# Kernel optimization log

Measured on AMD Instinct MI355X. Metric: run time of the kernel, lower is better.

Reference implementation:

```python
import jax, jax.numpy as jnp
import numpy as np

N_NODES = 10000
IN_CH = 512
HID = 128
HEADS = 4
OUT_CH = 256
N_EDGES = 160000
NEG_SLOPE = 0.2  # PyG GATConv default


def gat_conv(x, src, dst, W, a_src, a_dst, b):
    """PyG-style GATConv. x:[N,F_in], W:[F_in,H*C], a_src/a_dst:[H,C], b:[H*C].
    src/dst already include self-loops. Returns [N, H*C] (concat heads)."""
    N = x.shape[0]
    H, C = a_src.shape
    h = (x @ W).reshape(N, H, C)                     # [N,H,C]
    e_src = jnp.einsum('nhc,hc->nh', h, a_src)        # [N,H]
    e_dst = jnp.einsum('nhc,hc->nh', h, a_dst)
    alpha = jax.nn.leaky_relu(e_src[src] + e_dst[dst], NEG_SLOPE)  # [E,H]
    # softmax over incoming edges of each destination node
    m = jax.ops.segment_max(alpha, dst, num_segments=N)            # [N,H]
    ex = jnp.exp(alpha - m[dst])
    denom = jax.ops.segment_sum(ex, dst, num_segments=N)           # [N,H]
    coeff = ex / (denom[dst] + 1e-16)                              # [E,H]
    out = jax.ops.segment_sum(coeff[:, :, None] * h[src], dst, num_segments=N)  # [N,H,C]
    return out.reshape(N, H * C) + b


def _edges_with_self_loops(edge_index, n):
    loops = jnp.arange(n, dtype=edge_index.dtype)
    src = jnp.concatenate([edge_index[0], loops])
    dst = jnp.concatenate([edge_index[1], loops])
    return src, dst


def setup_inputs() -> dict:
    key = jax.random.key(0)
    ks = jax.random.split(key, 20)
    s = 0.05
    inp = {
        'x': jax.random.normal(ks[0], (N_NODES, IN_CH), jnp.float32),
        'W1': jax.random.normal(ks[1], (IN_CH, HEADS * HID), jnp.float32) * s,
        'a1s': jax.random.normal(ks[2], (HEADS, HID), jnp.float32) * s,
        'a1d': jax.random.normal(ks[3], (HEADS, HID), jnp.float32) * s,
        'b1': jnp.zeros((HEADS * HID,), jnp.float32),
        'W2': jax.random.normal(ks[4], (HEADS * HID, HEADS * HID), jnp.float32) * s,
        'a2s': jax.random.normal(ks[5], (HEADS, HID), jnp.float32) * s,
        'a2d': jax.random.normal(ks[6], (HEADS, HID), jnp.float32) * s,
        'b2': jnp.zeros((HEADS * HID,), jnp.float32),
        'W3': jax.random.normal(ks[7], (HEADS * HID, HID), jnp.float32) * s,
        'a3s': jax.random.normal(ks[8], (1, HID), jnp.float32) * s,
        'a3d': jax.random.normal(ks[9], (1, HID), jnp.float32) * s,
        'b3': jnp.zeros((HID,), jnp.float32),
        'Wl': jax.random.normal(ks[10], (HID, OUT_CH), jnp.float32) * s,
        'bl': jnp.zeros((OUT_CH,), jnp.float32),
        'Wr': jax.random.normal(ks[11], (IN_CH, OUT_CH), jnp.float32) * s,
        'br': jnp.zeros((OUT_CH,), jnp.float32),
        'edge_index': jax.random.randint(ks[12], (2, N_EDGES), 0, N_NODES, jnp.int64 if jax.config.jax_enable_x64 else jnp.int32),
    }
    return inp


def reference(x, W1, a1s, a1d, b1, W2, a2s, a2d, b2, W3, a3s, a3d, b3, Wl, bl, Wr, br, edge_index):
    src, dst = _edges_with_self_loops(edge_index, x.shape[0])
    residual = x @ Wr + br
    h = jax.nn.elu(gat_conv(x, src, dst, W1, a1s, a1d, b1))
    h = jax.nn.elu(gat_conv(h, src, dst, W2, a2s, a2d, b2))
    h = jax.nn.elu(gat_conv(h, src, dst, W3, a3s, a3d, b3))
    return h @ Wl + bl + residual
```

## Files before the change

### kernel.cpp

```cpp
#include <hip/hip_runtime.h>
#include <hip/hip_bf16.h>
#include <cstdint>
#include <cstddef>

#define N_NODES 10000
#define M_PAD   10112
#define HEADS   4

typedef __bf16 bfrag8 __attribute__((ext_vector_type(8)));
typedef __bf16 bfrag2 __attribute__((ext_vector_type(2)));
typedef float  floatx4 __attribute__((ext_vector_type(4)));

#define S0 (M_PAD * 512)
#define S1 (512 * 512)
#define S2 (512 * 512)
#define S3 (512 * 128)
#define S4 (128 * 256)
#define S5 (512 * 256)
#define SP_TOTAL (S0 + S1 + S2 + S3 + S4 + S5 + N_NODES)

__global__ __launch_bounds__(256) void prep(const float* __restrict__ x,
                                            const float* __restrict__ W1,
                                            const float* __restrict__ W2,
                                            const float* __restrict__ W3,
                                            const float* __restrict__ Wl,
                                            const float* __restrict__ Wr,
                                            __bf16* __restrict__ xb,
                                            __bf16* __restrict__ W1T,
                                            __bf16* __restrict__ W2T,
                                            __bf16* __restrict__ W3T,
                                            __bf16* __restrict__ WlT,
                                            __bf16* __restrict__ WrT,
                                            int* __restrict__ deg) {
    int i = blockIdx.x * 256 + threadIdx.x;
    if (i < S0) {
        int row = i >> 9;
        xb[i] = (row < N_NODES) ? (__bf16)x[i] : (__bf16)0.f;
    } else if ((i -= S0) < S1) {
        int k = i >> 9, n = i & 511;
        W1T[n * 512 + k] = (__bf16)W1[i];
    } else if ((i -= S1) < S2) {
        int k = i >> 9, n = i & 511;
        W2T[n * 512 + k] = (__bf16)W2[i];
    } else if ((i -= S2) < S3) {
        int k = i >> 7, n = i & 127;
        W3T[n * 512 + k] = (__bf16)W3[i];
    } else if ((i -= S3) < S4) {
        int k = i >> 8, n = i & 255;
        WlT[n * 128 + k] = (__bf16)Wl[i];
    } else if ((i -= S4) < S5) {
        int k = i >> 8, n = i & 255;
        WrT[n * 512 + k] = (__bf16)Wr[i];
    } else if ((i -= S5) < N_NODES) {
        deg[i] = 0;
    }
}


__global__ __launch_bounds__(256) void deg_kernel(const int* __restrict__ dst, int E,
                                                  int* __restrict__ deg) {
    int i = blockIdx.x * 256 + threadIdx.x;
    if (i < E) atomicAdd(&deg[dst[i]], 1);
}

__global__ __launch_bounds__(256) void scan_kernel(const int* __restrict__ deg,
                                                   int* __restrict__ rowptr,
                                                   int* __restrict__ cursor, int n) {
    __shared__ int wtot[4], woff[4];
    int t = threadIdx.x, lane = t & 63, wv = t >> 6;
    int chunk = (n + 255) / 256;
    int beg = t * chunk, end = beg + chunk; if (end > n) end = n; if (beg > n) beg = n;
    int s = 0;
    for (int i = beg; i < end; ++i) s += deg[i] + 1;
    int v = s;
#pragma unroll
    for (int off = 1; off < 64; off <<= 1) {
        int o = __shfl_up(v, off);
        if (lane >= off) v += o;
    }
    if (lane == 63) wtot[wv] = v;
    __syncthreads();
    if (t == 0) {
        int r = 0;
#pragma unroll
        for (int i = 0; i < 4; ++i) { woff[i] = r; r += wtot[i]; }
        rowptr[n] = r;
    }
    __syncthreads();
    int off = woff[wv] + v - s;
    for (int i = beg; i < end; ++i) {
        rowptr[i] = off; cursor[i] = off;
        off += deg[i] + 1;
    }
}

__global__ __launch_bounds__(256) void scatter_kernel(const int* __restrict__ src,
                                                      const int* __restrict__ dst, int E, int n,
                                                      int* __restrict__ cursor,
                                                      int* __restrict__ csr) {
    int i = blockIdx.x * 256 + threadIdx.x;
    if (i < E) {
        int pos = atomicAdd(&cursor[dst[i]], 1);
        csr[pos] = src[i];
    } else if (i < E + n) {
        int v = i - E;
        int pos = atomicAdd(&cursor[v], 1);
        csr[pos] = v;
    }
}


template <int NT>
__device__ __forceinline__ void gemm_loop(const __bf16* __restrict__ A,
                                          const __bf16* __restrict__ BT, int K,
                                          int m0, int n0, int wave, int lane,
                                          __bf16* As, __bf16* Bs,
                                          floatx4 (&acc)[2][NT]) {
    int r = wave * 8 + (lane >> 3);
    int kof = (lane & 7) * 8;
    const __bf16* gA = A + (size_t)(m0 + r) * K + kof;
    const __bf16* gB = BT + (size_t)(n0 + r) * K + kof;
    __bf16* lA = As + r * 64 + kof;
    __bf16* lB = Bs + r * 64 + kof;
    const __bf16* fA = As + (wave * 32 + (lane & 15)) * 64 + (lane >> 4) * 8;
    const __bf16* fB = Bs + (lane & 15) * 64 + (lane >> 4) * 8;

    for (int k0 = 0; k0 < K; k0 += 64) {
#pragma unroll
        for (int u = 0; u < 4; ++u)
            __builtin_amdgcn_global_load_lds(
                (const __attribute__((address_space(1))) void*)(gA + (size_t)u * 32 * K),
                (__attribute__((address_space(3))) void*)(lA + u * 32 * 64), 16, 0, 0);
#pragma unroll
        for (int u = 0; u < NT / 2; ++u)
            __builtin_amdgcn_global_load_lds(
                (const __attribute__((address_space(1))) void*)(gB + (size_t)u * 32 * K),
                (__attribute__((address_space(3))) void*)(lB + u * 32 * 64), 16, 0, 0);
        gA += 64; gB += 64;
        __syncthreads();

#pragma unroll
        for (int ks = 0; ks < 2; ++ks) {
            bfrag8 a0 = *(const bfrag8*)(fA + ks * 32);
            bfrag8 a1 = *(const bfrag8*)(fA + 16 * 64 + ks * 32);
#pragma unroll
            for (int nt = 0; nt < NT; ++nt) {
                bfrag8 b = *(const bfrag8*)(fB + nt * 16 * 64 + ks * 32);
                acc[0][nt] = __builtin_amdgcn_mfma_f32_16x16x32_bf16(a0, b, acc[0][nt], 0, 0, 0);
                acc[1][nt] = __builtin_amdgcn_mfma_f32_16x16x32_bf16(a1, b, acc[1][nt], 0, 0, 0);
            }
        }
        __syncthreads();
    }
}

__global__ __launch_bounds__(256) void gemm_h(const __bf16* __restrict__ A,
                                              const __bf16* __restrict__ BT,
                                              __bf16* __restrict__ Cb,
                                              int N, int K) {
    __shared__ __align__(16) __bf16 As[128 * 64];
    __shared__ __align__(16) __bf16 Bs[64 * 64];
    int tid = threadIdx.x, wave = tid >> 6, lane = tid & 63;
    int m0 = blockIdx.x * 128, n0 = blockIdx.y * 64;
    floatx4 acc[2][4] = {};
    gemm_loop<4>(A, BT, K, m0, n0, wave, lane, As, Bs, acc);

    int crow = m0 + wave * 32 + (lane >> 4) * 4;
    int ccol = n0 + (lane & 15);
#pragma unroll
    for (int mt = 0; mt < 2; ++mt)
#pragma unroll
        for (int nt = 0; nt < 4; ++nt)
#pragma unroll
            for (int r = 0; r < 4; ++r)
                Cb[(size_t)(crow + mt * 16 + r) * N + ccol + nt * 16] = (__bf16)acc[mt][nt][r];
}

__global__ __launch_bounds__(256) void gemm_final(const __bf16* __restrict__ A1,
                                                  const __bf16* __restrict__ B1T, int K1,
                                                  const __bf16* __restrict__ A2,
                                                  const __bf16* __restrict__ B2T, int K2,
                                                  float* __restrict__ C,
                                                  const float* __restrict__ bias1,
                                                  const float* __restrict__ bias2,
                                                  int M, int N) {
    __shared__ __align__(16) __bf16 As[128 * 64];
    __shared__ __align__(16) __bf16 Bs[64 * 64];
    int tid = threadIdx.x, wave = tid >> 6, lane = tid & 63;
    int m0 = blockIdx.x * 128, n0 = blockIdx.y * 64;
    floatx4 acc[2][4] = {};
    gemm_loop<4>(A1, B1T, K1, m0, n0, wave, lane, As, Bs, acc);
    gemm_loop<4>(A2, B2T, K2, m0, n0, wave, lane, As, Bs, acc);

    int crow = m0 + wave * 32 + (lane >> 4) * 4;
    int ccol = n0 + (lane & 15);
#pragma unroll
    for (int mt = 0; mt < 2; ++mt)
#pragma unroll
        for (int nt = 0; nt < 4; ++nt)
#pragma unroll
            for (int r = 0; r < 4; ++r) {
                int row = crow + mt * 16 + r;
                int col = ccol + nt * 16;
                if (row < M)
                    C[(size_t)row * N + col] = acc[mt][nt][r] + bias1[col] + bias2[col];
            }
}


template <int H>
__global__ __launch_bounds__(256) void attn_e(const __bf16* __restrict__ Hb,
                                              const float* __restrict__ as_,
                                              const float* __restrict__ ad_,
                                              float* __restrict__ es,
                                              float* __restrict__ ed) {
    constexpr int F = H * 128;
    constexpr int GROUP = (H == 4) ? 16 : 64;
    int wave = threadIdx.x >> 6, lane = threadIdx.x & 63;
    int node = blockIdx.x * 4 + wave;
    if (node >= N_NODES) return;
    float ps = 0.f, pd = 0.f;
    if (H == 4) {
        bfrag8 v = *(const bfrag8*)(Hb + (size_t)node * F + lane * 8);
#pragma unroll
        for (int k = 0; k < 8; ++k) {
            float f = (float)v[k];
            ps += f * as_[lane * 8 + k];
            pd += f * ad_[lane * 8 + k];
        }
    } else {
        bfrag2 v = *(const bfrag2*)(Hb + (size_t)node * F + lane * 2);
#pragma unroll
        for (int k = 0; k < 2; ++k) {
            float f = (float)v[k];
            ps += f * as_[lane * 2 + k];
            pd += f * ad_[lane * 2 + k];
        }
    }
#pragma unroll
    for (int off = GROUP / 2; off; off >>= 1) {
        ps += __shfl_down(ps, off);
        pd += __shfl_down(pd, off);
    }
    if ((lane & (GROUP - 1)) == 0) {
        es[node * H + lane / GROUP] = ps;
        ed[node * H + lane / GROUP] = pd;
    }
}


template <int H>
__global__ __launch_bounds__(256) void gather_agg(const __bf16* __restrict__ Hb,
                                                  const float* __restrict__ es,
                                                  const float* __restrict__ ed,
                                                  const int* __restrict__ rowptr,
                                                  const int* __restrict__ csr,
                                                  const float* __restrict__ bias,
                                                  __bf16* __restrict__ outb) {
    constexpr int F = H * 128;
    constexpr int CH = F / 64;
    int wave = threadIdx.x >> 6, lane = threadIdx.x & 63;
    int node = blockIdx.x * 4 + wave;
    if (node >= M_PAD) return;
    int hsel = (H == 4) ? (lane >> 4) : 0;
    __bf16* op = outb + (size_t)node * F + lane * CH;
    if (node >= N_NODES) {
        if (H == 4) { bfrag8 z = {}; *(bfrag8*)op = z; }
        else        { bfrag2 z = {}; *(bfrag2*)op = z; }
        return;
    }
    float edv = ed[node * H + hsel];
    int beg = rowptr[node], end = rowptr[node + 1];
    float acc[CH] = {};
    float wsum = 0.f;
    int j = beg;
    for (; j + 3 < end; j += 4) {
        int s0 = csr[j], s1 = csr[j + 1], s2 = csr[j + 2], s3 = csr[j + 3];
        float e0 = es[s0 * H + hsel], e1 = es[s1 * H + hsel];
        float e2 = es[s2 * H + hsel], e3 = es[s3 * H + hsel];
        if (H == 4) {
            bfrag8 h0 = *(const bfrag8*)(Hb + (size_t)s0 * F + lane * 8);
            bfrag8 h1 = *(const bfrag8*)(Hb + (size_t)s1 * F + lane * 8);
            bfrag8 h2 = *(const bfrag8*)(Hb + (size_t)s2 * F + lane * 8);
            bfrag8 h3 = *(const bfrag8*)(Hb + (size_t)s3 * F + lane * 8);
            e0 += edv; e1 += edv; e2 += edv; e3 += edv;
            e0 = e0 > 0.f ? e0 : 0.2f * e0;
            e1 = e1 > 0.f ? e1 : 0.2f * e1;
            e2 = e2 > 0.f ? e2 : 0.2f * e2;
            e3 = e3 > 0.f ? e3 : 0.2f * e3;
            float w0 = __expf(e0), w1 = __expf(e1), w2 = __expf(e2), w3 = __expf(e3);
            wsum += (w0 + w1) + (w2 + w3);
#pragma unroll
            for (int k = 0; k < 8; ++k)
                acc[k] += (w0 * (float)h0[k] + w1 * (float)h1[k]) +
                          (w2 * (float)h2[k] + w3 * (float)h3[k]);
        } else {
            bfrag2 h0 = *(const bfrag2*)(Hb + (size_t)s0 * F + lane * 2);
            bfrag2 h1 = *(const bfrag2*)(Hb + (size_t)s1 * F + lane * 2);
            bfrag2 h2 = *(const bfrag2*)(Hb + (size_t)s2 * F + lane * 2);
            bfrag2 h3 = *(const bfrag2*)(Hb + (size_t)s3 * F + lane * 2);
            e0 += edv; e1 += edv; e2 += edv; e3 += edv;
            e0 = e0 > 0.f ? e0 : 0.2f * e0;
            e1 = e1 > 0.f ? e1 : 0.2f * e1;
            e2 = e2 > 0.f ? e2 : 0.2f * e2;
            e3 = e3 > 0.f ? e3 : 0.2f * e3;
            float w0 = __expf(e0), w1 = __expf(e1), w2 = __expf(e2), w3 = __expf(e3);
            wsum += (w0 + w1) + (w2 + w3);
#pragma unroll
            for (int k = 0; k < 2; ++k)
                acc[k] += (w0 * (float)h0[k] + w1 * (float)h1[k]) +
                          (w2 * (float)h2[k] + w3 * (float)h3[k]);
        }
    }
    for (; j < end; ++j) {
        int s0 = csr[j];
        float e0 = es[s0 * H + hsel] + edv;
        e0 = e0 > 0.f ? e0 : 0.2f * e0;
        float w0 = __expf(e0);
        wsum += w0;
        if (H == 4) {
            bfrag8 h0 = *(const bfrag8*)(Hb + (size_t)s0 * F + lane * 8);
#pragma unroll
            for (int k = 0; k < 8; ++k) acc[k] += w0 * (float)h0[k];
        } else {
            bfrag2 h0 = *(const bfrag2*)(Hb + (size_t)s0 * F + lane * 2);
#pragma unroll
            for (int k = 0; k < 2; ++k) acc[k] += w0 * (float)h0[k];
        }
    }
    float inv = 1.f / (wsum + 1e-16f);
    if (H == 4) {
        bfrag8 r;
#pragma unroll
        for (int k = 0; k < 8; ++k) {
            float o = acc[k] * inv + bias[lane * 8 + k];
            o = o > 0.f ? o : __expf(o) - 1.f;
            r[k] = (__bf16)o;
        }
        *(bfrag8*)op = r;
    } else {
        bfrag2 r;
#pragma unroll
        for (int k = 0; k < 2; ++k) {
            float o = acc[k] * inv + bias[lane * 2 + k];
            o = o > 0.f ? o : __expf(o) - 1.f;
            r[k] = (__bf16)o;
        }
        *(bfrag2*)op = r;
    }
}


extern "C" void kernel_launch(void* const* d_in, const int* in_sizes, int n_in,
                              void* d_out, int out_size, void* d_ws, size_t ws_size,
                              hipStream_t stream) {
    const float* x   = (const float*)d_in[0];
    const float* W1  = (const float*)d_in[1];
    const float* a1s = (const float*)d_in[2];
    const float* a1d = (const float*)d_in[3];
    const float* b1  = (const float*)d_in[4];
    const float* W2  = (const float*)d_in[5];
    const float* a2s = (const float*)d_in[6];
    const float* a2d = (const float*)d_in[7];
    const float* b2  = (const float*)d_in[8];
    const float* W3  = (const float*)d_in[9];
    const float* a3s = (const float*)d_in[10];
    const float* a3d = (const float*)d_in[11];
    const float* b3  = (const float*)d_in[12];
    const float* Wl  = (const float*)d_in[13];
    const float* bl  = (const float*)d_in[14];
    const float* Wr  = (const float*)d_in[15];
    const float* br  = (const float*)d_in[16];
    const int*   ei  = (const int*)d_in[17];
    const int E = in_sizes[17] / 2;
    const int* esrc = ei;
    const int* edst = ei + E;
    const int slots = E + N_NODES;
    float* out = (float*)d_out;

    char* w = (char*)d_ws;
    auto alloc = [&](size_t b) { char* p = w; w += (b + 255) & ~(size_t)255; return p; };
    __bf16* xb  = (__bf16*)alloc((size_t)M_PAD * 512 * 2);
    __bf16* hb  = (__bf16*)alloc((size_t)M_PAD * 512 * 2);
    __bf16* hb3 = (__bf16*)alloc((size_t)M_PAD * 128 * 2);
    __bf16* Hib = (__bf16*)alloc((size_t)M_PAD * 512 * 2);
    __bf16* W1T = (__bf16*)alloc(512 * 512 * 2);
    __bf16* W2T = (__bf16*)alloc(512 * 512 * 2);
    __bf16* W3T = (__bf16*)alloc(128 * 512 * 2);
    __bf16* WlT = (__bf16*)alloc(256 * 128 * 2);
    __bf16* WrT = (__bf16*)alloc(256 * 512 * 2);
    float* es     = (float*)alloc(N_NODES * HEADS * 4);
    float* ed     = (float*)alloc(N_NODES * HEADS * 4);
    int*   deg    = (int*)alloc(N_NODES * 4);
    int*   rowptr = (int*)alloc((N_NODES + 1) * 4);
    int*   cursor = (int*)alloc(N_NODES * 4);
    int*   csr    = (int*)alloc((size_t)slots * 4);

    prep<<<(SP_TOTAL + 255) / 256, 256, 0, stream>>>(x, W1, W2, W3, Wl, Wr,
                                                     xb, W1T, W2T, W3T, WlT, WrT, deg);
    deg_kernel<<<(E + 255) / 256, 256, 0, stream>>>(edst, E, deg);
    scan_kernel<<<1, 256, 0, stream>>>(deg, rowptr, cursor, N_NODES);
    scatter_kernel<<<(E + N_NODES + 255) / 256, 256, 0, stream>>>(esrc, edst, E, N_NODES,
                                                                  cursor, csr);

    gemm_h<<<dim3(M_PAD / 128, 8), 256, 0, stream>>>(xb, W1T, Hib, 512, 512);
    attn_e<4><<<N_NODES / 4, 256, 0, stream>>>(Hib, a1s, a1d, es, ed);
    gather_agg<4><<<M_PAD / 4, 256, 0, stream>>>(Hib, es, ed, rowptr, csr, b1, hb);
    gemm_h<<<dim3(M_PAD / 128, 8), 256, 0, stream>>>(hb, W2T, Hib, 512, 512);
    attn_e<4><<<N_NODES / 4, 256, 0, stream>>>(Hib, a2s, a2d, es, ed);
    gather_agg<4><<<M_PAD / 4, 256, 0, stream>>>(Hib, es, ed, rowptr, csr, b2, hb);
    gemm_h<<<dim3(M_PAD / 128, 2), 256, 0, stream>>>(hb, W3T, Hib, 128, 512);
    attn_e<1><<<N_NODES / 4, 256, 0, stream>>>(Hib, a3s, a3d, es, ed);
    gather_agg<1><<<M_PAD / 4, 256, 0, stream>>>(Hib, es, ed, rowptr, csr, b3, hb3);
    gemm_final<<<dim3(M_PAD / 128, 4), 256, 0, stream>>>(xb, WrT, 512, hb3, WlT, 128,
                                                         out, br, bl, N_NODES, 256);
}
```

Before: 289.7 us.

## Fuse attention logits into GEMM epilogue, widen GEMM tiles, vectorize prep, unroll gather

Each GEMM block now covers a full 128-column head tile and computes the per-head source and destination attention logits in its epilogue with a shuffle reduction. This removes the separate attn_e kernels and their re-read of H. GEMM tiles widen from 64 to 128 columns and the grid is reordered so columns vary fastest. The x-to-bf16 conversion now converts 8 elements per thread with vector loads, and the gather loop unrolls 8 edges to keep more loads in flight. Larger accumulators raise register pressure, and the wider tiles give fewer blocks per GEMM.

```diff
diff --git a/kernel.cpp b/kernel.cpp
--- a/kernel.cpp
+++ b/kernel.cpp
@@ -11,13 +11,13 @@
 typedef __bf16 bfrag2 __attribute__((ext_vector_type(2)));
 typedef float  floatx4 __attribute__((ext_vector_type(4)));
 
-#define S0 (M_PAD * 512)
+#define S0V (M_PAD * 512 / 8)
 #define S1 (512 * 512)
 #define S2 (512 * 512)
 #define S3 (512 * 128)
 #define S4 (128 * 256)
 #define S5 (512 * 256)
-#define SP_TOTAL (S0 + S1 + S2 + S3 + S4 + S5 + N_NODES)
+#define SP_TOTAL (S0V + S1 + S2 + S3 + S4 + S5 + N_NODES)
 
 __global__ __launch_bounds__(256) void prep(const float* __restrict__ x,
                                             const float* __restrict__ W1,
@@ -33,10 +33,18 @@
                                             __bf16* __restrict__ WrT,
                                             int* __restrict__ deg) {
     int i = blockIdx.x * 256 + threadIdx.x;
-    if (i < S0) {
-        int row = i >> 9;
-        xb[i] = (row < N_NODES) ? (__bf16)x[i] : (__bf16)0.f;
-    } else if ((i -= S0) < S1) {
+    if (i < S0V) {
+        int base = i * 8;
+        int row = base >> 9;
+        bfrag8 r = {};
+        if (row < N_NODES) {
+            float4 f0 = ((const float4*)x)[i * 2];
+            float4 f1 = ((const float4*)x)[i * 2 + 1];
+            r[0] = (__bf16)f0.x; r[1] = (__bf16)f0.y; r[2] = (__bf16)f0.z; r[3] = (__bf16)f0.w;
+            r[4] = (__bf16)f1.x; r[5] = (__bf16)f1.y; r[6] = (__bf16)f1.z; r[7] = (__bf16)f1.w;
+        }
+        *(bfrag8*)(xb + base) = r;
+    } else if ((i -= S0V) < S1) {
         int k = i >> 9, n = i & 511;
         W1T[n * 512 + k] = (__bf16)W1[i];
     } else if ((i -= S1) < S2) {
@@ -157,23 +165,60 @@
 __global__ __launch_bounds__(256) void gemm_h(const __bf16* __restrict__ A,
                                               const __bf16* __restrict__ BT,
                                               __bf16* __restrict__ Cb,
-                                              int N, int K) {
+                                              int N, int K,
+                                              const float* __restrict__ as_,
+                                              const float* __restrict__ ad_,
+                                              float* __restrict__ es,
+                                              float* __restrict__ ed, int H) {
     __shared__ __align__(16) __bf16 As[128 * 64];
-    __shared__ __align__(16) __bf16 Bs[64 * 64];
+    __shared__ __align__(16) __bf16 Bs[128 * 64];
     int tid = threadIdx.x, wave = tid >> 6, lane = tid & 63;
-    int m0 = blockIdx.x * 128, n0 = blockIdx.y * 64;
-    floatx4 acc[2][4] = {};
-    gemm_loop<4>(A, BT, K, m0, n0, wave, lane, As, Bs, acc);
+    int n0 = blockIdx.x * 128, m0 = blockIdx.y * 128;
+    floatx4 acc[2][8] = {};
+    gemm_loop<8>(A, BT, K, m0, n0, wave, lane, As, Bs, acc);
 
     int crow = m0 + wave * 32 + (lane >> 4) * 4;
     int ccol = n0 + (lane & 15);
 #pragma unroll
     for (int mt = 0; mt < 2; ++mt)
 #pragma unroll
-        for (int nt = 0; nt < 4; ++nt)
+        for (int nt = 0; nt < 8; ++nt)
 #pragma unroll
             for (int r = 0; r < 4; ++r)
                 Cb[(size_t)(crow + mt * 16 + r) * N + ccol + nt * 16] = (__bf16)acc[mt][nt][r];
+
+    int head = blockIdx.x;
+    float a_sv[8], a_dv[8];
+#pragma unroll
+    for (int nt = 0; nt < 8; ++nt) {
+        int cin = nt * 16 + (lane & 15);
+        a_sv[nt] = as_[head * 128 + cin];
+        a_dv[nt] = ad_[head * 128 + cin];
+    }
+#pragma unroll
+    for (int mt = 0; mt < 2; ++mt)
+#pragma unroll
+        for (int r = 0; r < 4; ++r) {
+            float ps = 0.f, pd = 0.f;
+#pragma unroll
+            for (int nt = 0; nt < 8; ++nt) {
+                float v = acc[mt][nt][r];
+                ps += v * a_sv[nt];
+                pd += v * a_dv[nt];
+            }
+#pragma unroll
+            for (int off = 8; off; off >>= 1) {
+                ps += __shfl_xor(ps, off);
+                pd += __shfl_xor(pd, off);
+            }
+            if ((lane & 15) == 0) {
+                int row = crow + mt * 16 + r;
+                if (row < N_NODES) {
+                    es[row * H + head] = ps;
+                    ed[row * H + head] = pd;
+                }
+            }
+        }
 }
 
 __global__ __launch_bounds__(256) void gemm_final(const __bf16* __restrict__ A1,
@@ -185,19 +230,19 @@
                                                   const float* __restrict__ bias2,
                                                   int M, int N) {
     __shared__ __align__(16) __bf16 As[128 * 64];
-    __shared__ __align__(16) __bf16 Bs[64 * 64];
+    __shared__ __align__(16) __bf16 Bs[128 * 64];
     int tid = threadIdx.x, wave = tid >> 6, lane = tid & 63;
-    int m0 = blockIdx.x * 128, n0 = blockIdx.y * 64;
-    floatx4 acc[2][4] = {};
-    gemm_loop<4>(A1, B1T, K1, m0, n0, wave, lane, As, Bs, acc);
-    gemm_loop<4>(A2, B2T, K2, m0, n0, wave, lane, As, Bs, acc);
+    int n0 = blockIdx.x * 128, m0 = blockIdx.y * 128;
+    floatx4 acc[2][8] = {};
+    gemm_loop<8>(A1, B1T, K1, m0, n0, wave, lane, As, Bs, acc);
+    gemm_loop<8>(A2, B2T, K2, m0, n0, wave, lane, As, Bs, acc);
 
     int crow = m0 + wave * 32 + (lane >> 4) * 4;
     int ccol = n0 + (lane & 15);
 #pragma unroll
     for (int mt = 0; mt < 2; ++mt)
 #pragma unroll
-        for (int nt = 0; nt < 4; ++nt)
+        for (int nt = 0; nt < 8; ++nt)
 #pragma unroll
             for (int r = 0; r < 4; ++r) {
                 int row = crow + mt * 16 + r;
@@ -205,47 +250,6 @@
                 if (row < M)
                     C[(size_t)row * N + col] = acc[mt][nt][r] + bias1[col] + bias2[col];
             }
-}
-
-
-template <int H>
-__global__ __launch_bounds__(256) void attn_e(const __bf16* __restrict__ Hb,
-                                              const float* __restrict__ as_,
-                                              const float* __restrict__ ad_,
-                                              float* __restrict__ es,
-                                              float* __restrict__ ed) {
-    constexpr int F = H * 128;
-    constexpr int GROUP = (H == 4) ? 16 : 64;
-    int wave = threadIdx.x >> 6, lane = threadIdx.x & 63;
-    int node = blockIdx.x * 4 + wave;
-    if (node >= N_NODES) return;
-    float ps = 0.f, pd = 0.f;
-    if (H == 4) {
-        bfrag8 v = *(const bfrag8*)(Hb + (size_t)node * F + lane * 8);
-#pragma unroll
-        for (int k = 0; k < 8; ++k) {
-            float f = (float)v[k];
-            ps += f * as_[lane * 8 + k];
-            pd += f * ad_[lane * 8 + k];
-        }
-    } else {
-        bfrag2 v = *(const bfrag2*)(Hb + (size_t)node * F + lane * 2);
-#pragma unroll
-        for (int k = 0; k < 2; ++k) {
-            float f = (float)v[k];
-            ps += f * as_[lane * 2 + k];
-            pd += f * ad_[lane * 2 + k];
-        }
-    }
-#pragma unroll
-    for (int off = GROUP / 2; off; off >>= 1) {
-        ps += __shfl_down(ps, off);
-        pd += __shfl_down(pd, off);
-    }
-    if ((lane & (GROUP - 1)) == 0) {
-        es[node * H + lane / GROUP] = ps;
-        ed[node * H + lane / GROUP] = pd;
-    }
 }
 
 
@@ -274,42 +278,43 @@
     float acc[CH] = {};
     float wsum = 0.f;
     int j = beg;
-    for (; j + 3 < end; j += 4) {
-        int s0 = csr[j], s1 = csr[j + 1], s2 = csr[j + 2], s3 = csr[j + 3];
-        float e0 = es[s0 * H + hsel], e1 = es[s1 * H + hsel];
-        float e2 = es[s2 * H + hsel], e3 = es[s3 * H + hsel];
+    for (; j + 7 < end; j += 8) {
+        int s[8];
+        float e[8];
+#pragma unroll
+        for (int u = 0; u < 8; ++u) s[u] = csr[j + u];
+#pragma unroll
+        for (int u = 0; u < 8; ++u) e[u] = es[s[u] * H + hsel];
         if (H == 4) {
-            bfrag8 h0 = *(const bfrag8*)(Hb + (size_t)s0 * F + lane * 8);
-            bfrag8 h1 = *(const bfrag8*)(Hb + (size_t)s1 * F + lane * 8);
-            bfrag8 h2 = *(const bfrag8*)(Hb + (size_t)s2 * F + lane * 8);
-            bfrag8 h3 = *(const bfrag8*)(Hb + (size_t)s3 * F + lane * 8);
-            e0 += edv; e1 += edv; e2 += edv; e3 += edv;
-            e0 = e0 > 0.f ? e0 : 0.2f * e0;
-            e1 = e1 > 0.f ? e1 : 0.2f * e1;
-            e2 = e2 > 0.f ? e2 : 0.2f * e2;
-            e3 = e3 > 0.f ? e3 : 0.2f * e3;
-            float w0 = __expf(e0), w1 = __expf(e1), w2 = __expf(e2), w3 = __expf(e3);
-            wsum += (w0 + w1) + (w2 + w3);
-#pragma unroll
-            for (int k = 0; k < 8; ++k)
-                acc[k] += (w0 * (float)h0[k] + w1 * (float)h1[k]) +
-                          (w2 * (float)h2[k] + w3 * (float)h3[k]);
+            bfrag8 hv[8];
+#pragma unroll
+            for (int u = 0; u < 8; ++u) hv[u] = *(const bfrag8*)(Hb + (size_t)s[u] * F + lane * 8);
+#pragma unroll
+            for (int u = 0; u < 8; ++u) {
+                float t = e[u] + edv;
+                t = t > 0.f ? t : 0.2f * t;
+                e[u] = __expf(t);
+                wsum += e[u];
+            }
+#pragma unroll
+            for (int u = 0; u < 8; ++u)
+#pragma unroll
+                for (int k = 0; k < 8; ++k) acc[k] += e[u] * (float)hv[u][k];
         } else {
-            bfrag2 h0 = *(const bfrag2*)(Hb + (size_t)s0 * F + lane * 2);
-            bfrag2 h1 = *(const bfrag2*)(Hb + (size_t)s1 * F + lane * 2);
-            bfrag2 h2 = *(const bfrag2*)(Hb + (size_t)s2 * F + lane * 2);
-            bfrag2 h3 = *(const bfrag2*)(Hb + (size_t)s3 * F + lane * 2);
-            e0 += edv; e1 += edv; e2 += edv; e3 += edv;
-            e0 = e0 > 0.f ? e0 : 0.2f * e0;
-            e1 = e1 > 0.f ? e1 : 0.2f * e1;
-            e2 = e2 > 0.f ? e2 : 0.2f * e2;
-            e3 = e3 > 0.f ? e3 : 0.2f * e3;
-            float w0 = __expf(e0), w1 = __expf(e1), w2 = __expf(e2), w3 = __expf(e3);
-            wsum += (w0 + w1) + (w2 + w3);
-#pragma unroll
-            for (int k = 0; k < 2; ++k)
-                acc[k] += (w0 * (float)h0[k] + w1 * (float)h1[k]) +
-                          (w2 * (float)h2[k] + w3 * (float)h3[k]);
+            bfrag2 hv[8];
+#pragma unroll
+            for (int u = 0; u < 8; ++u) hv[u] = *(const bfrag2*)(Hb + (size_t)s[u] * F + lane * 2);
+#pragma unroll
+            for (int u = 0; u < 8; ++u) {
+                float t = e[u] + edv;
+                t = t > 0.f ? t : 0.2f * t;
+                e[u] = __expf(t);
+                wsum += e[u];
+            }
+#pragma unroll
+            for (int u = 0; u < 8; ++u)
+#pragma unroll
+                for (int k = 0; k < 2; ++k) acc[k] += e[u] * (float)hv[u][k];
         }
     }
     for (; j < end; ++j) {
@@ -403,15 +408,15 @@
     scatter_kernel<<<(E + N_NODES + 255) / 256, 256, 0, stream>>>(esrc, edst, E, N_NODES,
                                                                   cursor, csr);
 
-    gemm_h<<<dim3(M_PAD / 128, 8), 256, 0, stream>>>(xb, W1T, Hib, 512, 512);
-    attn_e<4><<<N_NODES / 4, 256, 0, stream>>>(Hib, a1s, a1d, es, ed);
+    gemm_h<<<dim3(4, M_PAD / 128), 256, 0, stream>>>(xb, W1T, Hib, 512, 512,
+                                                     a1s, a1d, es, ed, 4);
     gather_agg<4><<<M_PAD / 4, 256, 0, stream>>>(Hib, es, ed, rowptr, csr, b1, hb);
-    gemm_h<<<dim3(M_PAD / 128, 8), 256, 0, stream>>>(hb, W2T, Hib, 512, 512);
-    attn_e<4><<<N_NODES / 4, 256, 0, stream>>>(Hib, a2s, a2d, es, ed);
+    gemm_h<<<dim3(4, M_PAD / 128), 256, 0, stream>>>(hb, W2T, Hib, 512, 512,
+                                                     a2s, a2d, es, ed, 4);
     gather_agg<4><<<M_PAD / 4, 256, 0, stream>>>(Hib, es, ed, rowptr, csr, b2, hb);
-    gemm_h<<<dim3(M_PAD / 128, 2), 256, 0, stream>>>(hb, W3T, Hib, 128, 512);
-    attn_e<1><<<N_NODES / 4, 256, 0, stream>>>(Hib, a3s, a3d, es, ed);
+    gemm_h<<<dim3(1, M_PAD / 128), 256, 0, stream>>>(hb, W3T, Hib, 128, 512,
+                                                     a3s, a3d, es, ed, 1);
     gather_agg<1><<<M_PAD / 4, 256, 0, stream>>>(Hib, es, ed, rowptr, csr, b3, hb3);
-    gemm_final<<<dim3(M_PAD / 128, 4), 256, 0, stream>>>(xb, WrT, 512, hb3, WlT, 128,
+    gemm_final<<<dim3(2, M_PAD / 128), 256, 0, stream>>>(xb, WrT, 512, hb3, WlT, 128,
                                                          out, br, bl, N_NODES, 256);
 }
```

After: 292.3 us. About the same (+0.9%).

## Split gather per head, swap GEMM grid order, vectorize x conversion

Applied to the files above, without the earlier changes.

The 4-head neighbour aggregation is split into four separate launches, one per head. Each wave gathers 256 bytes per neighbour row (bf16x2 per lane), with 8 neighbours unrolled to keep more loads in flight. This is meant to shrink each launch's working set so it fits in cache. The GEMM grids now put the N-tile dimension on blockIdx.x so blocks sharing an A row-tile run close together, and the x-to-bf16 conversion in prep now uses float4 loads and 16-byte stores. The cost is more kernel launches, and the CSR and es data are re-read once per head.

```diff
diff --git a/kernel.cpp b/kernel.cpp
--- a/kernel.cpp
+++ b/kernel.cpp
@@ -11,13 +11,13 @@
 typedef __bf16 bfrag2 __attribute__((ext_vector_type(2)));
 typedef float  floatx4 __attribute__((ext_vector_type(4)));
 
-#define S0 (M_PAD * 512)
+#define S0V (M_PAD * 512 / 8)
 #define S1 (512 * 512)
 #define S2 (512 * 512)
 #define S3 (512 * 128)
 #define S4 (128 * 256)
 #define S5 (512 * 256)
-#define SP_TOTAL (S0 + S1 + S2 + S3 + S4 + S5 + N_NODES)
+#define SP_TOTAL (S0V + S1 + S2 + S3 + S4 + S5 + N_NODES)
 
 __global__ __launch_bounds__(256) void prep(const float* __restrict__ x,
                                             const float* __restrict__ W1,
@@ -33,10 +33,18 @@
                                             __bf16* __restrict__ WrT,
                                             int* __restrict__ deg) {
     int i = blockIdx.x * 256 + threadIdx.x;
-    if (i < S0) {
-        int row = i >> 9;
-        xb[i] = (row < N_NODES) ? (__bf16)x[i] : (__bf16)0.f;
-    } else if ((i -= S0) < S1) {
+    if (i < S0V) {
+        int base = i * 8;
+        int row = base >> 9;
+        bfrag8 r = {};
+        if (row < N_NODES) {
+            float4 f0 = ((const float4*)x)[i * 2];
+            float4 f1 = ((const float4*)x)[i * 2 + 1];
+            r[0] = (__bf16)f0.x; r[1] = (__bf16)f0.y; r[2] = (__bf16)f0.z; r[3] = (__bf16)f0.w;
+            r[4] = (__bf16)f1.x; r[5] = (__bf16)f1.y; r[6] = (__bf16)f1.z; r[7] = (__bf16)f1.w;
+        }
+        *(bfrag8*)(xb + base) = r;
+    } else if ((i -= S0V) < S1) {
         int k = i >> 9, n = i & 511;
         W1T[n * 512 + k] = (__bf16)W1[i];
     } else if ((i -= S1) < S2) {
@@ -161,7 +169,7 @@
     __shared__ __align__(16) __bf16 As[128 * 64];
     __shared__ __align__(16) __bf16 Bs[64 * 64];
     int tid = threadIdx.x, wave = tid >> 6, lane = tid & 63;
-    int m0 = blockIdx.x * 128, n0 = blockIdx.y * 64;
+    int n0 = blockIdx.x * 64, m0 = blockIdx.y * 128;
     floatx4 acc[2][4] = {};
     gemm_loop<4>(A, BT, K, m0, n0, wave, lane, As, Bs, acc);
 
@@ -187,7 +195,7 @@
     __shared__ __align__(16) __bf16 As[128 * 64];
     __shared__ __align__(16) __bf16 Bs[64 * 64];
     int tid = threadIdx.x, wave = tid >> 6, lane = tid & 63;
-    int m0 = blockIdx.x * 128, n0 = blockIdx.y * 64;
+    int n0 = blockIdx.x * 64, m0 = blockIdx.y * 128;
     floatx4 acc[2][4] = {};
     gemm_loop<4>(A1, B1T, K1, m0, n0, wave, lane, As, Bs, acc);
     gemm_loop<4>(A2, B2T, K2, m0, n0, wave, lane, As, Bs, acc);
@@ -250,104 +258,68 @@
 
 
 template <int H>
-__global__ __launch_bounds__(256) void gather_agg(const __bf16* __restrict__ Hb,
-                                                  const float* __restrict__ es,
-                                                  const float* __restrict__ ed,
-                                                  const int* __restrict__ rowptr,
-                                                  const int* __restrict__ csr,
-                                                  const float* __restrict__ bias,
-                                                  __bf16* __restrict__ outb) {
+__global__ __launch_bounds__(256) void gather_head(const __bf16* __restrict__ Hb,
+                                                   const float* __restrict__ es,
+                                                   const float* __restrict__ ed,
+                                                   const int* __restrict__ rowptr,
+                                                   const int* __restrict__ csr,
+                                                   const float* __restrict__ bias,
+                                                   __bf16* __restrict__ outb,
+                                                   int head) {
     constexpr int F = H * 128;
-    constexpr int CH = F / 64;
     int wave = threadIdx.x >> 6, lane = threadIdx.x & 63;
     int node = blockIdx.x * 4 + wave;
     if (node >= M_PAD) return;
-    int hsel = (H == 4) ? (lane >> 4) : 0;
-    __bf16* op = outb + (size_t)node * F + lane * CH;
+    __bf16* op = outb + (size_t)node * F + head * 128 + lane * 2;
     if (node >= N_NODES) {
-        if (H == 4) { bfrag8 z = {}; *(bfrag8*)op = z; }
-        else        { bfrag2 z = {}; *(bfrag2*)op = z; }
+        bfrag2 z = {};
+        *(bfrag2*)op = z;
         return;
     }
-    float edv = ed[node * H + hsel];
+    const __bf16* hp = Hb + head * 128 + lane * 2;
+    float edv = ed[node * H + head];
     int beg = rowptr[node], end = rowptr[node + 1];
-    float acc[CH] = {};
-    float wsum = 0.f;
+    float a0 = 0.f, a1 = 0.f, wsum = 0.f;
     int j = beg;
-    for (; j + 3 < end; j += 4) {
-        int s0 = csr[j], s1 = csr[j + 1], s2 = csr[j + 2], s3 = csr[j + 3];
-        float e0 = es[s0 * H + hsel], e1 = es[s1 * H + hsel];
-        float e2 = es[s2 * H + hsel], e3 = es[s3 * H + hsel];
-        if (H == 4) {
-            bfrag8 h0 = *(const bfrag8*)(Hb + (size_t)s0 * F + lane * 8);
-            bfrag8 h1 = *(const bfrag8*)(Hb + (size_t)s1 * F + lane * 8);
-            bfrag8 h2 = *(const bfrag8*)(Hb + (size_t)s2 * F + lane * 8);
-            bfrag8 h3 = *(const bfrag8*)(Hb + (size_t)s3 * F + lane * 8);
-            e0 += edv; e1 += edv; e2 += edv; e3 += edv;
-            e0 = e0 > 0.f ? e0 : 0.2f * e0;
-            e1 = e1 > 0.f ? e1 : 0.2f * e1;
-            e2 = e2 > 0.f ? e2 : 0.2f * e2;
-            e3 = e3 > 0.f ? e3 : 0.2f * e3;
-            float w0 = __expf(e0), w1 = __expf(e1), w2 = __expf(e2), w3 = __expf(e3);
-            wsum += (w0 + w1) + (w2 + w3);
-#pragma unroll
-            for (int k = 0; k < 8; ++k)
-                acc[k] += (w0 * (float)h0[k] + w1 * (float)h1[k]) +
-                          (w2 * (float)h2[k] + w3 * (float)h3[k]);
-        } else {
-            bfrag2 h0 = *(const bfrag2*)(Hb + (size_t)s0 * F + lane * 2);
-            bfrag2 h1 = *(const bfrag2*)(Hb + (size_t)s1 * F + lane * 2);
-            bfrag2 h2 = *(const bfrag2*)(Hb + (size_t)s2 * F + lane * 2);
-            bfrag2 h3 = *(const bfrag2*)(Hb + (size_t)s3 * F + lane * 2);
-            e0 += edv; e1 += edv; e2 += edv; e3 += edv;
-            e0 = e0 > 0.f ? e0 : 0.2f * e0;
-            e1 = e1 > 0.f ? e1 : 0.2f * e1;
-            e2 = e2 > 0.f ? e2 : 0.2f * e2;
-            e3 = e3 > 0.f ? e3 : 0.2f * e3;
-            float w0 = __expf(e0), w1 = __expf(e1), w2 = __expf(e2), w3 = __expf(e3);
-            wsum += (w0 + w1) + (w2 + w3);
-#pragma unroll
-            for (int k = 0; k < 2; ++k)
-                acc[k] += (w0 * (float)h0[k] + w1 * (float)h1[k]) +
-                          (w2 * (float)h2[k] + w3 * (float)h3[k]);
+    for (; j + 7 < end; j += 8) {
+        int s[8];
+        float e[8];
+        bfrag2 hv[8];
+#pragma unroll
+        for (int u = 0; u < 8; ++u) s[u] = csr[j + u];
+#pragma unroll
+        for (int u = 0; u < 8; ++u) e[u] = es[s[u] * H + head];
+#pragma unroll
+        for (int u = 0; u < 8; ++u) hv[u] = *(const bfrag2*)(hp + (size_t)s[u] * F);
+#pragma unroll
+        for (int u = 0; u < 8; ++u) {
+            float t = e[u] + edv;
+            t = t > 0.f ? t : 0.2f * t;
+            float wgt = __expf(t);
+            wsum += wgt;
+            a0 += wgt * (float)hv[u][0];
+            a1 += wgt * (float)hv[u][1];
         }
     }
     for (; j < end; ++j) {
         int s0 = csr[j];
-        float e0 = es[s0 * H + hsel] + edv;
-        e0 = e0 > 0.f ? e0 : 0.2f * e0;
-        float w0 = __expf(e0);
-        wsum += w0;
-        if (H == 4) {
-            bfrag8 h0 = *(const bfrag8*)(Hb + (size_t)s0 * F + lane * 8);
-#pragma unroll
-            for (int k = 0; k < 8; ++k) acc[k] += w0 * (float)h0[k];
-        } else {
-            bfrag2 h0 = *(const bfrag2*)(Hb + (size_t)s0 * F + lane * 2);
-#pragma unroll
-            for (int k = 0; k < 2; ++k) acc[k] += w0 * (float)h0[k];
-        }
+        float t = es[s0 * H + head] + edv;
+        t = t > 0.f ? t : 0.2f * t;
+        float wgt = __expf(t);
+        wsum += wgt;
+        bfrag2 hv = *(const bfrag2*)(hp + (size_t)s0 * F);
+        a0 += wgt * (float)hv[0];
+        a1 += wgt * (float)hv[1];
     }
     float inv = 1.f / (wsum + 1e-16f);
-    if (H == 4) {
-        bfrag8 r;
-#pragma unroll
-        for (int k = 0; k < 8; ++k) {
-            float o = acc[k] * inv + bias[lane * 8 + k];
-            o = o > 0.f ? o : __expf(o) - 1.f;
-            r[k] = (__bf16)o;
-        }
-        *(bfrag8*)op = r;
-    } else {
-        bfrag2 r;
-#pragma unroll
-        for (int k = 0; k < 2; ++k) {
-            float o = acc[k] * inv + bias[lane * 2 + k];
-            o = o > 0.f ? o : __expf(o) - 1.f;
-            r[k] = (__bf16)o;
-        }
-        *(bfrag2*)op = r;
-    }
+    float o0 = a0 * inv + bias[head * 128 + lane * 2];
+    float o1 = a1 * inv + bias[head * 128 + lane * 2 + 1];
+    o0 = o0 > 0.f ? o0 : __expf(o0) - 1.f;
+    o1 = o1 > 0.f ? o1 : __expf(o1) - 1.f;
+    bfrag2 r;
+    r[0] = (__bf16)o0;
+    r[1] = (__bf16)o1;
+    *(bfrag2*)op = r;
 }
 
 
@@ -403,15 +375,17 @@
     scatter_kernel<<<(E + N_NODES + 255) / 256, 256, 0, stream>>>(esrc, edst, E, N_NODES,
                                                                   cursor, csr);
 
-    gemm_h<<<dim3(M_PAD / 128, 8), 256, 0, stream>>>(xb, W1T, Hib, 512, 512);
+    gemm_h<<<dim3(8, M_PAD / 128), 256, 0, stream>>>(xb, W1T, Hib, 512, 512);
     attn_e<4><<<N_NODES / 4, 256, 0, stream>>>(Hib, a1s, a1d, es, ed);
-    gather_agg<4><<<M_PAD / 4, 256, 0, stream>>>(Hib, es, ed, rowptr, csr, b1, hb);
-    gemm_h<<<dim3(M_PAD / 128, 8), 256, 0, stream>>>(hb, W2T, Hib, 512, 512);
+    for (int h = 0; h < 4; ++h)
+        gather_head<4><<<M_PAD / 4, 256, 0, stream>>>(Hib, es, ed, rowptr, csr, b1, hb, h);
+    gemm_h<<<dim3(8, M_PAD / 128), 256, 0, stream>>>(hb, W2T, Hib, 512, 512);
     attn_e<4><<<N_NODES / 4, 256, 0, stream>>>(Hib, a2s, a2d, es, ed);
-    gather_agg<4><<<M_PAD / 4, 256, 0, stream>>>(Hib, es, ed, rowptr, csr, b2, hb);
-    gemm_h<<<dim3(M_PAD / 128, 2), 256, 0, stream>>>(hb, W3T, Hib, 128, 512);
+    for (int h = 0; h < 4; ++h)
+        gather_head<4><<<M_PAD / 4, 256, 0, stream>>>(Hib, es, ed, rowptr, csr, b2, hb, h);
+    gemm_h<<<dim3(2, M_PAD / 128), 256, 0, stream>>>(hb, W3T, Hib, 128, 512);
     attn_e<1><<<N_NODES / 4, 256, 0, stream>>>(Hib, a3s, a3d, es, ed);
-    gather_agg<1><<<M_PAD / 4, 256, 0, stream>>>(Hib, es, ed, rowptr, csr, b3, hb3);
-    gemm_final<<<dim3(M_PAD / 128, 4), 256, 0, stream>>>(xb, WrT, 512, hb3, WlT, 128,
+    gather_head<1><<<M_PAD / 4, 256, 0, stream>>>(Hib, es, ed, rowptr, csr, b3, hb3, 0);
+    gemm_final<<<dim3(4, M_PAD / 128), 256, 0, stream>>>(xb, WrT, 512, hb3, WlT, 128,
                                                          out, br, bl, N_NODES, 256);
 }
```

Result: slower. 329.6 us (+13.8%).
